# Kernel tuning notes

Hardware: AMD Instinct MI355X
Metric: run time of the kernel (lower is better)

The kernel has to match this reference:

```python
import jax, jax.numpy as jnp
import numpy as np

B, N, DPOS, F, P, K = 32, 1024, 3, 64, 128, 16


def setup_inputs() -> dict:
    key = jax.random.key(0)
    kp, kf, kw1, kw2 = jax.random.split(key, 4)
    points = jax.random.normal(kp, (B, N, DPOS), dtype=jnp.float32)
    features = jax.random.normal(kf, (B, N, F), dtype=jnp.float32)
    W1 = jax.random.normal(kw1, (2 * F, 2 * P), dtype=jnp.float32) * (1.0 / np.sqrt(2 * F))
    b1 = jnp.zeros((2 * P,), dtype=jnp.float32)
    W2 = jax.random.normal(kw2, (2 * P, P), dtype=jnp.float32) * (1.0 / np.sqrt(2 * P))
    b2 = jnp.zeros((P,), dtype=jnp.float32)
    return {"points": points, "features": features, "W1": W1, "b1": b1, "W2": W2, "b2": b2}


def reference(points, features, W1, b1, W2, b2):
    # pairwise squared distances: r_i - 2 p_i.p_j + r_j + 1e-5  -> [B, N, N]
    r = jnp.sum(points * points, axis=2, keepdims=True)
    m = jnp.einsum('bnd,bmd->bnm', points, points)
    D = r - 2.0 * m + jnp.swapaxes(r, 1, 2) + 1e-5
    # K+1 nearest (incl. self), drop self -> indices [B, N, K]
    _, idx = jax.lax.top_k(-D, K + 1)
    idx = idx[:, :, 1:]
    # gather neighbor features: [B, N, K, F]
    neighbors = features[jnp.arange(B)[:, None, None], idx]
    center = jnp.broadcast_to(features[:, :, None, :], neighbors.shape)
    local = jnp.concatenate([neighbors - center, center], axis=-1)  # [B,N,K,2F]
    # 2-layer MLP with exact GELU
    h = jax.nn.gelu(jnp.einsum('bnkf,fh->bnkh', local, W1) + b1, approximate=False)
    out = jax.nn.gelu(jnp.einsum('bnkh,hp->bnkp', h, W2) + b2, approximate=False)
    # mean over neighbors -> [B, N, P]
    return jnp.mean(out, axis=2)
```

## Files before the change

### kernel.cpp

```cpp
#include <hip/hip_runtime.h>
#include <math.h>

#define BB 32
#define NN 1024
#define FF 64
#define PP 128
#define KNN 16
#define H2 256
#define F2 128
#define KSEL 17
#define SVCAP 272

typedef float f32x4 __attribute__((ext_vector_type(4)));
typedef _Float16 f16x8 __attribute__((ext_vector_type(8)));
typedef _Float16 f16x4 __attribute__((ext_vector_type(4)));
typedef _Float16 f16x2 __attribute__((ext_vector_type(2)));

#define GC1 0.39616247f
#define GC3 -0.05891477f
#define GC5 0.00563735f
#define GC7 -2.10439e-4f
#define GXC 3.2988f

__device__ __forceinline__ f16x8 splat8(float f) {
    _Float16 h = (_Float16)f;
    f16x8 v = {h, h, h, h, h, h, h, h};
    return v;
}
__device__ __forceinline__ f16x4 splat4(float f) {
    _Float16 h = (_Float16)f;
    f16x4 v = {h, h, h, h};
    return v;
}

__device__ __forceinline__ f16x8 act8(f16x8 gv, f16x8 qv) {
    const f16x8 XL = splat8(-GXC), XH = splat8(GXC);
    const f16x8 C1 = splat8(GC1), C3 = splat8(GC3), C5 = splat8(GC5), C7 = splat8(GC7);
    const f16x8 HF = splat8(0.5f);
    f16x8 x  = gv + qv;
    f16x8 xc = __builtin_elementwise_min(__builtin_elementwise_max(x, XL), XH);
    f16x8 s  = xc * xc;
    f16x8 t  = s * C7 + C5;
    t = s * t + C3;
    t = s * t + C1;
    f16x8 u = xc * t + HF;
    return x * u;
}

__device__ __forceinline__ float gelu4_sum(f32x4 a, float bias) {
    f16x4 x;
    x[0] = (_Float16)(a[0] + bias);
    x[1] = (_Float16)(a[1] + bias);
    x[2] = (_Float16)(a[2] + bias);
    x[3] = (_Float16)(a[3] + bias);
    const f16x4 XL = splat4(-GXC), XH = splat4(GXC);
    const f16x4 C1 = splat4(GC1), C3 = splat4(GC3), C5 = splat4(GC5), C7 = splat4(GC7);
    const f16x4 HF = splat4(0.5f);
    f16x4 xc = __builtin_elementwise_min(__builtin_elementwise_max(x, XL), XH);
    f16x4 s  = xc * xc;
    f16x4 t  = s * C7 + C5;
    t = s * t + C3;
    t = s * t + C1;
    f16x4 u = xc * t + HF;
    f16x4 y = x * u;
    f16x2 y2 = __builtin_shufflevector(y, y, 0, 1) + __builtin_shufflevector(y, y, 2, 3);
    return (float)y2[0] + (float)y2[1];
}

__global__ __launch_bounds__(512) void prep_weights(const float* __restrict__ W1,
                                                    const float* __restrict__ W2,
                                                    _Float16* __restrict__ Wcf,
                                                    _Float16* __restrict__ W2f) {
    int tid = blockIdx.x * 512 + threadIdx.x;
    if (tid < 4096) {
        const int lane = tid & 63, quad = lane >> 4, l16 = lane & 15;
        const int kk = (tid >> 6) & 1, n_tile = tid >> 7;
        const int n = n_tile * 16 + l16;
        const int kb = kk * 32 + quad * 8;
        f16x8 v;
#pragma unroll
        for (int j = 0; j < 8; ++j) {
            const int k = kb + j;
            float x = (n < 256) ? W1[k * 256 + n]
                                : (W1[(64 + k) * 256 + (n - 256)] - W1[k * 256 + (n - 256)]);
            v[j] = (_Float16)x;
        }
        *(f16x8*)(Wcf + (size_t)tid * 8) = v;
    } else {
        const int t2 = tid - 4096;
        const int lane = t2 & 63, quad = lane >> 4, l16 = lane & 15;
        const int nt = (t2 >> 6) & 7, kk8 = t2 >> 9;
        const int p = nt * 16 + l16;
        const int hb = kk8 * 32 + quad * 8;
        f16x8 v;
#pragma unroll
        for (int j = 0; j < 8; ++j) v[j] = (_Float16)W2[(size_t)(hb + j) * PP + p];
        *(f16x8*)(W2f + (size_t)t2 * 8) = v;
    }
}

__global__ __launch_bounds__(512, 8) void knn_gq(const float* __restrict__ points,
                                                 int* __restrict__ idx_out,
                                                 const float* __restrict__ feat,
                                                 const _Float16* __restrict__ Wcf,
                                                 const float* __restrict__ b1,
                                                 _Float16* __restrict__ Gall,
                                                 _Float16* __restrict__ Qall) {
    __shared__ __align__(16) unsigned char smem[35840];
    const int t = threadIdx.x;

    if (blockIdx.x >= 4096) {
        _Float16 (*st)[16][136] = (_Float16(*)[16][136])smem;
        const int w8 = t >> 6, lane = t & 63;
        const int w4 = w8 & 3;
        const int quad = lane >> 4, l16 = lane & 15;
        const int gb = blockIdx.x - 4096;
        const int gbl = ((gb & 7) << 7) | (gb >> 3);
        const int m0 = gbl * 32 + (w8 >> 2) * 16;

        f16x8 a[2];
#pragma unroll
        for (int kk = 0; kk < 2; ++kk) {
            const float* ap = feat + (size_t)(m0 + l16) * 64 + kk * 32 + quad * 8;
            float4 a0 = *(const float4*)ap, a1 = *(const float4*)(ap + 4);
            f16x8 v;
            v[0] = (_Float16)a0.x; v[1] = (_Float16)a0.y; v[2] = (_Float16)a0.z; v[3] = (_Float16)a0.w;
            v[4] = (_Float16)a1.x; v[5] = (_Float16)a1.y; v[6] = (_Float16)a1.z; v[7] = (_Float16)a1.w;
            a[kk] = v;
        }
        f32x4 acc[8];
#pragma unroll
        for (int nt = 0; nt < 8; ++nt) acc[nt] = (f32x4){0.f, 0.f, 0.f, 0.f};
#pragma unroll
        for (int kk = 0; kk < 2; ++kk)
#pragma unroll
            for (int nt = 0; nt < 8; ++nt) {
                f16x8 bf = *(const f16x8*)(Wcf + (size_t)(((w4 * 8 + nt) * 2 + kk) * 64 + lane) * 8);
                acc[nt] = __builtin_amdgcn_mfma_f32_16x16x32_f16(a[kk], bf, acc[nt], 0, 0, 0);
            }

        const bool isQ = (w4 >= 2);
#pragma unroll
        for (int nt = 0; nt < 8; ++nt) {
            const int col = nt * 16 + l16;
            const float bias = isQ ? b1[(w4 - 2) * 128 + col] : 0.f;
#pragma unroll
            for (int r = 0; r < 4; ++r)
                st[w8][quad * 4 + r][col] = (_Float16)(acc[nt][r] + bias);
        }
        __syncthreads();

        const int row = lane >> 2, c = lane & 3;
        const int m = m0 + row;
#pragma unroll
        for (int i = 0; i < 4; ++i) {
            const int col = c * 32 + i * 8;
            f16x8 v = *(const f16x8*)&st[w8][row][col];
            if (!isQ) *(f16x8*)(Gall + (size_t)m * H2 + w4 * 128 + col) = v;
            else      *(f16x8*)(Qall + (size_t)m * H2 + (w4 - 2) * 128 + col) = v;
        }
        return;
    }

    float2* pxy = (float2*)smem;
    float2* pzr = (float2*)(smem + 8192);
    unsigned (*sv_val)[SVCAP] = (unsigned(*)[SVCAP])(smem + 16384);
    unsigned (*sv_idx)[SVCAP] = (unsigned(*)[SVCAP])(smem + 25088);
    unsigned (*tie_idx)[64]   = (unsigned(*)[64])(smem + 33792);

    const int lbk = ((blockIdx.x & 7) << 9) | (blockIdx.x >> 3);

    const int w = t >> 6, lane = t & 63;
    const int b = lbk >> 7;
    const int q0 = (lbk & 127) * 8;
    const float* pb = points + (size_t)b * NN * 3;
    const unsigned long long lt = (1ull << lane) - 1ull;

    for (int i = t; i < NN; i += 512) {
        float x = pb[3 * i], y = pb[3 * i + 1], z = pb[3 * i + 2];
        float r = __fadd_rn(__fadd_rn(__fmul_rn(x, x), __fmul_rn(y, y)), __fmul_rn(z, z));
        pxy[i] = make_float2(x, y);
        pzr[i] = make_float2(z, r);
    }
    __syncthreads();

    const int qn = q0 + w;
    const int gq = b * NN + qn;
    const float2 qv1 = pxy[qn], qv2 = pzr[qn];
    const float qx = qv1.x, qy = qv1.y, qz = qv2.x, qw = qv2.y;

    float D[16];
#pragma unroll
    for (int j = 0; j < 16; ++j) {
        const int m = j * 64 + lane;
        const float2 v1 = pxy[m], v2 = pzr[m];
        float dot = __fadd_rn(__fadd_rn(__fmul_rn(qx, v1.x), __fmul_rn(qy, v1.y)),
                              __fmul_rn(qz, v2.x));
        D[j] = __fadd_rn(__fadd_rn(__fsub_rn(qw, __fmul_rn(2.0f, dot)), v2.y), 1e-5f);
    }

    float mnf = D[0];
#pragma unroll
    for (int j = 1; j < 16; ++j) mnf = fminf(mnf, D[j]);
    const unsigned mbits = __float_as_uint(mnf);

    const unsigned mhi = mbits >> 16;
    unsigned Thi = 0;
#pragma unroll
    for (int bit = 15; bit >= 0; --bit) {
        unsigned cand = Thi | (1u << bit);
        int cnt = __popcll(__ballot(mhi < cand));
        if (cnt < KSEL) Thi = cand;
    }
    const unsigned T = (Thi << 16) | 0xFFFFu;

    unsigned base = 0;
#pragma unroll
    for (int j = 0; j < 16; ++j) {
        unsigned vb = __float_as_uint(D[j]);
        bool keep = (vb <= T);
        unsigned long long m = __ballot(keep);
        if (keep) {
            unsigned pos = base + (unsigned)__popcll(m & lt);
            if (pos < SVCAP) { sv_val[w][pos] = vb; sv_idx[w][pos] = j * 64 + lane; }
        }
        base += (unsigned)__popcll(m);
    }
    unsigned C = base > SVCAP ? SVCAP : base;

    unsigned rv[5], ri[5];
#pragma unroll
    for (int s = 0; s < 5; ++s) {
        int i = s * 64 + lane;
        bool ok = (i < (int)C);
        rv[s] = ok ? sv_val[w][i] : 0xFFFFFFFFu;
        ri[s] = ok ? sv_idx[w][i] : 0xFFFFFFFFu;
    }

    unsigned Ts = 0;
    if (C <= 64) {
#pragma unroll
        for (int bit = 31; bit >= 0; --bit) {
            unsigned cand = Ts | (1u << bit);
            int cnt = __popcll(__ballot(rv[0] < cand));
            if (cnt < KSEL) Ts = cand;
        }
    } else {
#pragma unroll
        for (int bit = 31; bit >= 0; --bit) {
            unsigned cand = Ts | (1u << bit);
            int cnt = 0;
#pragma unroll
            for (int s = 0; s < 5; ++s)
                cnt += __popcll(__ballot(rv[s] < cand));
            if (cnt < KSEL) Ts = cand;
        }
    }

    int L = 0;
#pragma unroll
    for (int s = 0; s < 5; ++s) L += __popcll(__ballot(rv[s] < Ts));
    const int need = KSEL - L;

    unsigned vmin_l = 0xFFFFFFFFu;
#pragma unroll
    for (int s = 0; s < 5; ++s) vmin_l = vmin_l < rv[s] ? vmin_l : rv[s];
#pragma unroll
    for (int off = 32; off >= 1; off >>= 1) {
        unsigned o2 = __shfl_xor(vmin_l, off, 64);
        vmin_l = vmin_l < o2 ? vmin_l : o2;
    }
    const unsigned Vmin = vmin_l;
    unsigned imin_l = 0xFFFFFFFFu;
#pragma unroll
    for (int s = 0; s < 5; ++s)
        if (rv[s] == Vmin && ri[s] < imin_l) imin_l = ri[s];
#pragma unroll
    for (int off = 32; off >= 1; off >>= 1) {
        unsigned o2 = __shfl_xor(imin_l, off, 64);
        imin_l = imin_l < o2 ? imin_l : o2;
    }
    const unsigned dropIdx = imin_l;

    int* o = idx_out + (size_t)gq * KNN;
    unsigned wbase = 0, tbase = 0;
#pragma unroll
    for (int s = 0; s < 5; ++s) {
        unsigned vb = rv[s], mi = ri[s];
        bool wk = (vb < Ts) && (mi != dropIdx);
        unsigned long long wm = __ballot(wk);
        if (wk) o[wbase + (unsigned)__popcll(wm & lt)] = (int)mi;
        wbase += (unsigned)__popcll(wm);
        bool tk = (vb == Ts);
        unsigned long long tm2 = __ballot(tk);
        if (tk) {
            unsigned tp = tbase + (unsigned)__popcll(tm2 & lt);
            if (tp < 64) tie_idx[w][tp] = mi;
        }
        tbase += (unsigned)__popcll(tm2);
    }
    unsigned tc = tbase > 64 ? 64 : tbase;
    if ((int)tc == need) {
        bool tk = (lane < (int)tc);
        unsigned mi2 = tk ? tie_idx[w][lane] : 0xFFFFFFFFu;
        tk = tk && (mi2 != dropIdx);
        unsigned long long m3 = __ballot(tk);
        if (tk) o[wbase + (unsigned)__popcll(m3 & lt)] = (int)mi2;
    } else if (lane == 0) {
        unsigned pos = wbase;
        for (int r = 0; r < need; ++r) {
            unsigned best = 0xFFFFFFFFu; int bj = 0;
            for (int j2 = 0; j2 < (int)tc; ++j2) {
                unsigned mi = tie_idx[w][j2];
                if (mi < best) { best = mi; bj = j2; }
            }
            tie_idx[w][bj] = 0xFFFFFFFFu;
            if (best != dropIdx) o[pos++] = (int)best;
        }
    }
}

__global__ __launch_bounds__(512, 3) void fused_mlp16(const _Float16* __restrict__ Gall,
                                                      const _Float16* __restrict__ Qall,
                                                      const int* __restrict__ knn_idx,
                                                      const _Float16* __restrict__ W2f,
                                                      const float* __restrict__ b2,
                                                      float* __restrict__ out) {
    __shared__ __align__(16) _Float16 w2s[32768];
    const int t = threadIdx.x, w = t >> 6, lane = t & 63;
    const int quad = lane >> 4, l16 = lane & 15;

    const int lb = ((blockIdx.x & 7) << 8) | (blockIdx.x >> 3);

    const int q0 = lb * 16 + w * 2;
    const int b = q0 >> 10;
    const int nb0 = knn_idx[q0 * KNN + l16];
    const int nb1 = knn_idx[(q0 + 1) * KNN + l16];
    const _Float16* g0 = Gall + ((size_t)(b << 10) + nb0) * H2;
    const _Float16* g1 = Gall + ((size_t)(b << 10) + nb1) * H2;
    const _Float16* qq0 = Qall + (size_t)q0 * H2;
    const _Float16* qq1 = qq0 + H2;

#pragma unroll
    for (int i = 0; i < 8; ++i) {
        f16x8 v = *(const f16x8*)(W2f + (size_t)(i * 4096 + t * 8));
        *(f16x8*)&w2s[i * 4096 + t * 8] = v;
    }

    f32x4 acc[2][8];
#pragma unroll
    for (int tm = 0; tm < 2; ++tm)
#pragma unroll
        for (int nt = 0; nt < 8; ++nt) acc[tm][nt] = (f32x4){0.f, 0.f, 0.f, 0.f};

    __syncthreads();

#pragma unroll
    for (int rk = 0; rk < 8; ++rk) {
        const int ho = rk * 32 + quad * 8;
        f16x8 gA = *(const f16x8*)(g0 + ho);
        f16x8 qA = *(const f16x8*)(qq0 + ho);
        f16x8 gB = *(const f16x8*)(g1 + ho);
        f16x8 qB = *(const f16x8*)(qq1 + ho);
        f16x8 a0 = act8(gA, qA);
        f16x8 a1 = act8(gB, qB);
        const _Float16* bb = &w2s[rk * 4096 + lane * 8];
#pragma unroll
        for (int nt = 0; nt < 8; ++nt) {
            f16x8 bf = *(const f16x8*)(bb + nt * 512);
            acc[0][nt] = __builtin_amdgcn_mfma_f32_16x16x32_f16(a0, bf, acc[0][nt], 0, 0, 0);
            acc[1][nt] = __builtin_amdgcn_mfma_f32_16x16x32_f16(a1, bf, acc[1][nt], 0, 0, 0);
        }
    }

    __syncthreads();
    float* obuf = (float*)w2s;
#pragma unroll
    for (int tm = 0; tm < 2; ++tm)
#pragma unroll
        for (int nt = 0; nt < 8; ++nt) {
            const float bias = b2[nt * 16 + l16];
            float s = gelu4_sum(acc[tm][nt], bias);
            s += __shfl_xor(s, 16, 64);
            s += __shfl_xor(s, 32, 64);
            if (quad == 0)
                obuf[(w * 2 + tm) * 128 + nt * 16 + l16] = s * 0.0625f;
        }
    __syncthreads();
    {
        float4 v = *(const float4*)&obuf[t * 4];
        *(float4*)(out + (size_t)lb * 2048 + t * 4) = v;
    }
}

extern "C" void kernel_launch(void* const* d_in, const int* in_sizes, int n_in,
                              void* d_out, int out_size, void* d_ws, size_t ws_size,
                              hipStream_t stream) {
    const float* points   = (const float*)d_in[0];
    const float* features = (const float*)d_in[1];
    const float* W1 = (const float*)d_in[2];
    const float* b1 = (const float*)d_in[3];
    const float* W2 = (const float*)d_in[4];
    const float* b2 = (const float*)d_in[5];
    float* out = (float*)d_out;

    const size_t IDX_B  = (size_t)BB * NN * KNN * 4;
    const size_t WCF_B  = 512 * 64 * 2;
    const size_t W2F_B  = 256 * 128 * 2;
    const size_t G_B    = (size_t)BB * NN * H2 * 2;

    int* knn_idx = (int*)d_ws;
    char* p = (char*)d_ws + IDX_B;
    _Float16* Wcf  = (_Float16*)p;  p += WCF_B;
    _Float16* W2f  = (_Float16*)p;  p += W2F_B;
    _Float16* Gall = (_Float16*)p;  p += G_B;
    _Float16* Qall = (_Float16*)p;

    prep_weights<<<16, 512, 0, stream>>>(W1, W2, Wcf, W2f);
    knn_gq<<<5120, 512, 0, stream>>>(points, knn_idx, features, Wcf, b1, Gall, Qall);
    fused_mlp16<<<2048, 512, 0, stream>>>(Gall, Qall, knn_idx, W2f, b2, out);
}
```

Before: 188.2 us.

## Stream G/Q rows and W2 halves into LDS with async global_load_lds double-buffering

Rewrites the fused MLP kernel so neighbor G rows, the Q rows and W2 are fetched with global_load_lds, which copies global memory straight into LDS. G chunks are double-buffered, and manual vmcnt waits let each chunk's load overlap the MFMA work on the previous chunk. W2 is staged in two halves with extra barriers in between. The goal is to hide global gather latency behind compute, at the cost of more LDS per block (72KB total, up from 64KB), two extra barriers, and reliance on hand-written waitcnt ordering.

```diff
diff --git a/kernel.cpp b/kernel.cpp
--- a/kernel.cpp
+++ b/kernel.cpp
@@ -67,6 +67,12 @@
     return (float)y2[0] + (float)y2[1];
 }
 
+__device__ __forceinline__ void gld16(const void* g, void* l) {
+    __builtin_amdgcn_global_load_lds((const __attribute__((address_space(1))) unsigned int*)g,
+                                     (__attribute__((address_space(3))) unsigned int*)l,
+                                     16, 0, 0);
+}
+
 __global__ __launch_bounds__(512) void prep_weights(const float* __restrict__ W1,
                                                     const float* __restrict__ W2,
                                                     _Float16* __restrict__ Wcf,
@@ -320,13 +326,15 @@
     }
 }
 
-__global__ __launch_bounds__(512, 3) void fused_mlp16(const _Float16* __restrict__ Gall,
+__global__ __launch_bounds__(512, 3) void fused_mlp17(const _Float16* __restrict__ Gall,
                                                       const _Float16* __restrict__ Qall,
                                                       const int* __restrict__ knn_idx,
                                                       const _Float16* __restrict__ W2f,
                                                       const float* __restrict__ b2,
                                                       float* __restrict__ out) {
-    __shared__ __align__(16) _Float16 w2s[32768];
+    __shared__ __align__(16) _Float16 w2s[16384];
+    __shared__ __align__(16) _Float16 gbuf[8][2][1024];
+    __shared__ __align__(16) _Float16 qbuf[8][512];
     const int t = threadIdx.x, w = t >> 6, lane = t & 63;
     const int quad = lane >> 4, l16 = lane & 15;
 
@@ -338,14 +346,20 @@
     const int nb1 = knn_idx[(q0 + 1) * KNN + l16];
     const _Float16* g0 = Gall + ((size_t)(b << 10) + nb0) * H2;
     const _Float16* g1 = Gall + ((size_t)(b << 10) + nb1) * H2;
-    const _Float16* qq0 = Qall + (size_t)q0 * H2;
-    const _Float16* qq1 = qq0 + H2;
-
-#pragma unroll
-    for (int i = 0; i < 8; ++i) {
-        f16x8 v = *(const f16x8*)(W2f + (size_t)(i * 4096 + t * 8));
-        *(f16x8*)&w2s[i * 4096 + t * 8] = v;
-    }
+
+    const char* aG0 = (const char*)g0 + quad * 16;
+    const char* aG1 = (const char*)g1 + quad * 16;
+    const char* aQ  = (const char*)(Qall + (size_t)q0 * H2) + (lane >> 5) * (H2 * 2) + (lane & 31) * 16;
+    const char* w2b = (const char*)W2f;
+
+    gld16(aQ, &qbuf[w][0]);
+#pragma unroll
+    for (int i = 0; i < 4; ++i)
+        gld16(w2b + i * 8192 + w * 1024 + lane * 16, &w2s[i * 4096 + w * 512]);
+    gld16(aG0,      &gbuf[w][0][0]);
+    gld16(aG1,      &gbuf[w][0][512]);
+    gld16(aG0 + 64, &gbuf[w][1][0]);
+    gld16(aG1 + 64, &gbuf[w][1][512]);
 
     f32x4 acc[2][8];
 #pragma unroll
@@ -355,23 +369,38 @@
 
     __syncthreads();
 
-#pragma unroll
-    for (int rk = 0; rk < 8; ++rk) {
-        const int ho = rk * 32 + quad * 8;
-        f16x8 gA = *(const f16x8*)(g0 + ho);
-        f16x8 qA = *(const f16x8*)(qq0 + ho);
-        f16x8 gB = *(const f16x8*)(g1 + ho);
-        f16x8 qB = *(const f16x8*)(qq1 + ho);
-        f16x8 a0 = act8(gA, qA);
-        f16x8 a1 = act8(gB, qB);
-        const _Float16* bb = &w2s[rk * 4096 + lane * 8];
-#pragma unroll
-        for (int nt = 0; nt < 8; ++nt) {
-            f16x8 bf = *(const f16x8*)(bb + nt * 512);
-            acc[0][nt] = __builtin_amdgcn_mfma_f32_16x16x32_f16(a0, bf, acc[0][nt], 0, 0, 0);
-            acc[1][nt] = __builtin_amdgcn_mfma_f32_16x16x32_f16(a1, bf, acc[1][nt], 0, 0, 0);
-        }
-    }
+#define STEP(RK, WN)                                                                   \
+    {                                                                                  \
+        asm volatile("s_waitcnt vmcnt(%c0)" ::"i"(WN) : "memory");                     \
+        f16x8 gA = *(const f16x8*)&gbuf[w][(RK) & 1][lane * 8];                        \
+        f16x8 gB = *(const f16x8*)&gbuf[w][(RK) & 1][512 + lane * 8];                  \
+        f16x8 qA = *(const f16x8*)&qbuf[w][(RK) * 32 + quad * 8];                      \
+        f16x8 qB = *(const f16x8*)&qbuf[w][256 + (RK) * 32 + quad * 8];                \
+        f16x8 a0 = act8(gA, qA);                                                       \
+        f16x8 a1 = act8(gB, qB);                                                       \
+        if ((RK) < 6) {                                                                \
+            gld16(aG0 + ((RK) + 2) * 64, &gbuf[w][(RK) & 1][0]);                       \
+            gld16(aG1 + ((RK) + 2) * 64, &gbuf[w][(RK) & 1][512]);                     \
+        }                                                                              \
+        const _Float16* bb = &w2s[((RK) & 3) * 4096 + lane * 8];                       \
+        _Pragma("unroll")                                                              \
+        for (int nt = 0; nt < 8; ++nt) {                                               \
+            f16x8 bf = *(const f16x8*)(bb + nt * 512);                                 \
+            acc[0][nt] = __builtin_amdgcn_mfma_f32_16x16x32_f16(a0, bf, acc[0][nt], 0, 0, 0); \
+            acc[1][nt] = __builtin_amdgcn_mfma_f32_16x16x32_f16(a1, bf, acc[1][nt], 0, 0, 0); \
+        }                                                                              \
+    }
+
+    STEP(0, 2) STEP(1, 2) STEP(2, 2) STEP(3, 2)
+
+    __syncthreads();
+#pragma unroll
+    for (int i = 0; i < 4; ++i)
+        gld16(w2b + 32768 + i * 8192 + w * 1024 + lane * 16, &w2s[i * 4096 + w * 512]);
+    __syncthreads();
+
+    STEP(4, 2) STEP(5, 2) STEP(6, 2) STEP(7, 0)
+#undef STEP
 
     __syncthreads();
     float* obuf = (float*)w2s;
@@ -418,5 +447,5 @@
 
     prep_weights<<<16, 512, 0, stream>>>(W1, W2, Wcf, W2f);
     knn_gq<<<5120, 512, 0, stream>>>(points, knn_idx, features, Wcf, b1, Gall, Qall);
-    fused_mlp16<<<2048, 512, 0, stream>>>(Gall, Qall, knn_idx, W2f, b2, out);
-}
+    fused_mlp17<<<2048, 512, 0, stream>>>(Gall, Qall, knn_idx, W2f, b2, out);
+}
```

New measurement: 184.5 us. 2.0% less time.
